# Kernel tuning notes

Measured on AMD Instinct MI355X. Metric: run time of the kernel, lower is better.

The kernel has to match this reference:

```python
import jax, jax.numpy as jnp
import numpy as np

H = 4096
DFF = 16384
EPS = 1e-5

def _layernorm(x, gamma, beta, eps):
    mu = jnp.mean(x, axis=-1, keepdims=True)
    var = jnp.var(x, axis=-1, keepdims=True)
    return (x - mu) * jax.lax.rsqrt(var + eps) * gamma + beta

def setup_inputs() -> dict:
    key = jax.random.key(0)
    ks = jax.random.split(key, 9)
    B, S = 2, 2048
    s_h = 1.0 / np.sqrt(H)
    s_f = 1.0 / np.sqrt(DFF)
    return {
        "input": jax.random.normal(ks[0], (B, S, H), jnp.float32),
        "residual": jax.random.normal(ks[1], (B, S, H), jnp.float32),
        "residual_norm": jax.random.normal(ks[2], (B, S, H), jnp.float32),
        "bias": jax.random.normal(ks[3], (H,), jnp.float32) * 0.02,
        "attn_nw": 1.0 + jax.random.normal(ks[4], (H,), jnp.float32) * 0.02,
        "attn_nb": jax.random.normal(ks[5], (H,), jnp.float32) * 0.02,
        "inter_w": jax.random.normal(ks[6], (H, DFF), jnp.float32) * s_h,
        "inter_b": jax.random.normal(ks[7], (DFF,), jnp.float32) * 0.02,
        "output_w": jax.random.normal(ks[8], (DFF, H), jnp.float32) * s_f,
        "output_b": jnp.zeros((H,), jnp.float32),
    }

def reference(input, residual, residual_norm, bias, attn_nw, attn_nb,
              inter_w, inter_b, output_w, output_b):
    # mlp_gemm (pre_layer_norm, mlp_after_attn, fp32, no quant):
    # LN(input + residual + attn_bias) -> GEMM -> GeLU -> GEMM
    ln_in = input + residual + bias                      # [B,S,H]
    ln = _layernorm(ln_in, attn_nw, attn_nb, EPS)        # [B,S,H]
    inter = jax.nn.gelu(jnp.einsum('bsh,hf->bsf', ln, inter_w) + inter_b,
                        approximate=True)                # [B,S,DFF]
    out = jnp.einsum('bsf,fh->bsh', inter, output_w)     # [B,S,H]
    # residual_add (preln, add_bias, mp_size=1):
    # residual = mlp_out + residual + attn_out + (attn_bias + mlp_bias)/mp_size
    return out + residual + input + (bias + output_b)
```

## Files before the change

kernel.cpp:

```cpp
#include <hip/hip_runtime.h>
#include <cstdint>
#include <cstddef>

#define H_DIM 4096
#define DFF_DIM 16384
#define NROWS 4096

typedef unsigned short bf16_t;
typedef __attribute__((ext_vector_type(8))) short bf16x8;
typedef __attribute__((ext_vector_type(4))) float f32x4;
typedef __attribute__((ext_vector_type(4))) unsigned short u16x4;

static __device__ __forceinline__ bf16_t f2bf(float f) {
  union { float f; unsigned int i; } v; v.f = f;
  unsigned int x = v.i;
  return (bf16_t)((x + 0x7fffu + ((x >> 16) & 1u)) >> 16);
}

#define GLDS16(gp, lp)                                                    \
  __builtin_amdgcn_global_load_lds(                                       \
      (__attribute__((address_space(1))) void*)(gp),                      \
      (__attribute__((address_space(3))) void*)(lp), 16, 0, 0)

__global__ __launch_bounds__(256) void fused_ln_kernel(
    const float* __restrict__ inp, const float* __restrict__ res,
    const float* __restrict__ bias, const float* __restrict__ gamma,
    const float* __restrict__ beta, bf16_t* __restrict__ out) {
  int row = blockIdx.x;
  int t = threadIdx.x;
  const float4* pin = (const float4*)(inp + (size_t)row * H_DIM);
  const float4* pre = (const float4*)(res + (size_t)row * H_DIM);
  const float4* pbi = (const float4*)bias;
  float4 xv[4];
  float s = 0.f, ss = 0.f;
#pragma unroll
  for (int i = 0; i < 4; ++i) {
    int idx = t + i * 256;
    float4 a = pin[idx];
    float4 b = pre[idx];
    float4 c = pbi[idx];
    float4 v;
    v.x = a.x + b.x + c.x;
    v.y = a.y + b.y + c.y;
    v.z = a.z + b.z + c.z;
    v.w = a.w + b.w + c.w;
    xv[i] = v;
    s += v.x + v.y + v.z + v.w;
    ss += v.x * v.x + v.y * v.y + v.z * v.z + v.w * v.w;
  }
#pragma unroll
  for (int off = 32; off > 0; off >>= 1) {
    s += __shfl_xor(s, off);
    ss += __shfl_xor(ss, off);
  }
  __shared__ float sred[8];
  int w = t >> 6, l = t & 63;
  if (l == 0) { sred[w] = s; sred[4 + w] = ss; }
  __syncthreads();
  s = sred[0] + sred[1] + sred[2] + sred[3];
  ss = sred[4] + sred[5] + sred[6] + sred[7];
  const float inv = 1.f / (float)H_DIM;
  float mean = s * inv;
  float var = ss * inv - mean * mean;
  float rstd = rsqrtf(var + 1e-5f);
  const float4* pg = (const float4*)gamma;
  const float4* pb = (const float4*)beta;
#pragma unroll
  for (int i = 0; i < 4; ++i) {
    int idx = t + i * 256;
    float4 g = pg[idx];
    float4 bb = pb[idx];
    float4 v = xv[i];
    u16x4 o;
    o.x = f2bf((v.x - mean) * rstd * g.x + bb.x);
    o.y = f2bf((v.y - mean) * rstd * g.y + bb.y);
    o.z = f2bf((v.z - mean) * rstd * g.z + bb.z);
    o.w = f2bf((v.w - mean) * rstd * g.w + bb.w);
    *(u16x4*)(out + (size_t)row * H_DIM + (size_t)idx * 4) = o;
  }
}

__global__ __launch_bounds__(256) void transpose_cvt_kernel(
    const float* __restrict__ W, bf16_t* __restrict__ Wt, int K, int N) {
  __shared__ float tile[64][65];
  int nb = N >> 6;
  int bk = blockIdx.x / nb;
  int bn = blockIdx.x - bk * nb;
  int t = threadIdx.x;
  int r = t >> 4;
  int c4 = (t & 15) << 2;
#pragma unroll
  for (int p = 0; p < 4; ++p) {
    int row = r + p * 16;
    float4 v = *(const float4*)(W + (size_t)(bk * 64 + row) * N + bn * 64 + c4);
    tile[row][c4 + 0] = v.x;
    tile[row][c4 + 1] = v.y;
    tile[row][c4 + 2] = v.z;
    tile[row][c4 + 3] = v.w;
  }
  __syncthreads();
#pragma unroll
  for (int p = 0; p < 4; ++p) {
    int nn = r + p * 16;
    u16x4 o;
    o.x = f2bf(tile[c4 + 0][nn]);
    o.y = f2bf(tile[c4 + 1][nn]);
    o.z = f2bf(tile[c4 + 2][nn]);
    o.w = f2bf(tile[c4 + 3][nn]);
    *(u16x4*)(Wt + (size_t)(bn * 64 + nn) * K + bk * 64 + c4) = o;
  }
}

#define QMFMA_H(AQ, BQ, MILO, NJLO, K5)                                     \
  __builtin_amdgcn_s_setprio(1);                                            \
  _Pragma("unroll") for (int i5 = 0; i5 < 4; ++i5)                          \
  _Pragma("unroll") for (int j5 = 0; j5 < 2; ++j5)                          \
    acc[MILO + i5][NJLO + j5] = __builtin_amdgcn_mfma_f32_16x16x32_bf16(    \
        AQ[i5 * 2 + K5], BQ[j5 * 2 + K5], acc[MILO + i5][NJLO + j5], 0, 0, 0); \
  __builtin_amdgcn_s_setprio(0);

#define BAR __builtin_amdgcn_s_barrier()
#define VM6 asm volatile("s_waitcnt vmcnt(6)" ::: "memory")

template <int EPI>
__global__ __launch_bounds__(512, 2) void gemm8p_kernel(
    const bf16_t* __restrict__ A, const bf16_t* __restrict__ Bt,
    int M, int N, int K,
    const float* __restrict__ eb1, const float* __restrict__ eb2,
    const float* __restrict__ add1, const float* __restrict__ add2,
    bf16_t* __restrict__ outb, float* __restrict__ outf) {
  __shared__ char lds[131072];

  const int t = threadIdx.x;
  const int l = t & 63;
  const int wid = t >> 6;
  const int wr = wid >> 2;
  const int wc = wid & 3;

  int nwg = gridDim.x;
  int bid = blockIdx.x;
  int wg = (bid & 7) * (nwg >> 3) + (bid >> 3);
  int ntm = M >> 8;
  int chunk = wg >> 5, s5 = wg & 31;
  int cmn = ntm >> 3;
  int cm = chunk % cmn, cn = chunk / cmn;
  int tm = cm * 8 + (s5 & 7);
  int tn = cn * 4 + (s5 >> 3);
  size_t m0 = (size_t)tm * 256, n0 = (size_t)tn * 256;

  f32x4 acc[8][4];
#pragma unroll
  for (int i = 0; i < 8; ++i)
#pragma unroll
    for (int j = 0; j < 4; ++j) acc[i][j] = {0.f, 0.f, 0.f, 0.f};

  const int rh = t >> 3;
  const int sl = t & 7;
  const int oc = sl ^ ((rh >> 1) & 7);
  const bf16_t* sA0 = A + (m0 + rh) * (size_t)K + oc * 8;
  const bf16_t* sA1 = A + (m0 + rh + 64) * (size_t)K + oc * 8;
  const bf16_t* sB0 = Bt + (n0 + rh) * (size_t)K + oc * 8;
  const bf16_t* sB1 = Bt + (n0 + rh + 64) * (size_t)K + oc * 8;

  auto stA = [&](int b, int h, int T) {
    GLDS16(sA0 + (size_t)h * 128 * K + (size_t)T * 64,
           lds + b * 32768 + h * 16384 + t * 16);
    GLDS16(sA1 + (size_t)h * 128 * K + (size_t)T * 64,
           lds + b * 32768 + h * 16384 + (t + 512) * 16);
  };
  auto stB = [&](int b, int h, int T) {
    GLDS16(sB0 + (size_t)h * 128 * K + (size_t)T * 64,
           lds + 65536 + b * 32768 + h * 16384 + t * 16);
    GLDS16(sB1 + (size_t)h * 128 * K + (size_t)T * 64,
           lds + 65536 + b * 32768 + h * 16384 + (t + 512) * 16);
  };

  int offA[8][2], offB[4][2];
#pragma unroll
  for (int mi = 0; mi < 8; ++mi) {
    int h = mi >> 2;
    int lr = (mi & 3) * 32 + wr * 16 + (l & 15);
#pragma unroll
    for (int ks = 0; ks < 2; ++ks) {
      int o = ks * 4 + (l >> 4);
      offA[mi][ks] = h * 16384 + lr * 128 + ((o ^ ((lr >> 1) & 7)) << 4);
    }
  }
#pragma unroll
  for (int nj = 0; nj < 4; ++nj) {
    int h = nj >> 1;
    int lc = (nj & 1) * 64 + wc * 16 + (l & 15);
#pragma unroll
    for (int ks = 0; ks < 2; ++ks) {
      int o = ks * 4 + (l >> 4);
      offB[nj][ks] = 65536 + h * 16384 + lc * 128 + ((o ^ ((lc >> 1) & 7)) << 4);
    }
  }

  auto rd8 = [&](int off) -> bf16x8 {
    return *(const bf16x8*)(const void*)(lds + off);
  };

  const int NT = K >> 6;
  const int NI = NT >> 1;

  stB(0, 0, 0); stA(0, 0, 0); stB(0, 1, 0); stA(0, 1, 0);
  stB(1, 0, 1); stA(1, 0, 1); stB(1, 1, 1);
  VM6;
  BAR;

  bf16x8 aQ[8], bQ0[4], bQ1[4];
#pragma unroll
  for (int i = 0; i < 4; ++i)
#pragma unroll
    for (int ks = 0; ks < 2; ++ks) aQ[i * 2 + ks] = rd8(offA[i][ks]);
#pragma unroll
  for (int j = 0; j < 2; ++j)
#pragma unroll
    for (int ks = 0; ks < 2; ++ks) bQ0[j * 2 + ks] = rd8(offB[j][ks]);

  for (int it = 0; it < NI; ++it) {
    const int Tb = 2 * it + 1;
    int Sa = 2 * it + 2; if (Sa >= NT) Sa = NT - 1;
    int Sb = 2 * it + 3; if (Sb >= NT) Sb = NT - 1;

    stA(1, 1, Tb);
    BAR;
    QMFMA_H(aQ, bQ0, 0, 0, 0)
    bQ1[0] = rd8(offB[2][0]); bQ1[2] = rd8(offB[3][0]);
    QMFMA_H(aQ, bQ0, 0, 0, 1)
    bQ1[1] = rd8(offB[2][1]); bQ1[3] = rd8(offB[3][1]);
    BAR;
    stB(0, 0, Sa);
    BAR;
    QMFMA_H(aQ, bQ1, 0, 2, 0)
    aQ[0] = rd8(offA[4][0]); aQ[2] = rd8(offA[5][0]);
    aQ[4] = rd8(offA[6][0]); aQ[6] = rd8(offA[7][0]);
    QMFMA_H(aQ, bQ1, 0, 2, 1)
    aQ[1] = rd8(offA[4][1]); aQ[3] = rd8(offA[5][1]);
    aQ[5] = rd8(offA[6][1]); aQ[7] = rd8(offA[7][1]);
    BAR;
    stA(0, 0, Sa);
    BAR;
    QMFMA_H(aQ, bQ1, 4, 2, 0)
    QMFMA_H(aQ, bQ1, 4, 2, 1)
    BAR;
    stB(0, 1, Sa);
    VM6;
    BAR;
    QMFMA_H(aQ, bQ0, 4, 0, 0)
    bQ0[0] = rd8(32768 + offB[0][0]); bQ0[2] = rd8(32768 + offB[1][0]);
    aQ[0] = rd8(32768 + offA[0][0]); aQ[2] = rd8(32768 + offA[1][0]);
    aQ[4] = rd8(32768 + offA[2][0]); aQ[6] = rd8(32768 + offA[3][0]);
    QMFMA_H(aQ, bQ0, 4, 0, 1)
    bQ0[1] = rd8(32768 + offB[0][1]); bQ0[3] = rd8(32768 + offB[1][1]);
    aQ[1] = rd8(32768 + offA[0][1]); aQ[3] = rd8(32768 + offA[1][1]);
    aQ[5] = rd8(32768 + offA[2][1]); aQ[7] = rd8(32768 + offA[3][1]);
    BAR;

    stA(0, 1, Sa);
    BAR;
    QMFMA_H(aQ, bQ0, 0, 0, 0)
    bQ1[0] = rd8(32768 + offB[2][0]); bQ1[2] = rd8(32768 + offB[3][0]);
    QMFMA_H(aQ, bQ0, 0, 0, 1)
    bQ1[1] = rd8(32768 + offB[2][1]); bQ1[3] = rd8(32768 + offB[3][1]);
    BAR;
    stB(1, 0, Sb);
    BAR;
    QMFMA_H(aQ, bQ1, 0, 2, 0)
    aQ[0] = rd8(32768 + offA[4][0]); aQ[2] = rd8(32768 + offA[5][0]);
    aQ[4] = rd8(32768 + offA[6][0]); aQ[6] = rd8(32768 + offA[7][0]);
    QMFMA_H(aQ, bQ1, 0, 2, 1)
    aQ[1] = rd8(32768 + offA[4][1]); aQ[3] = rd8(32768 + offA[5][1]);
    aQ[5] = rd8(32768 + offA[6][1]); aQ[7] = rd8(32768 + offA[7][1]);
    BAR;
    stA(1, 0, Sb);
    BAR;
    QMFMA_H(aQ, bQ1, 4, 2, 0)
    QMFMA_H(aQ, bQ1, 4, 2, 1)
    BAR;
    stB(1, 1, Sb);
    VM6;
    BAR;
    QMFMA_H(aQ, bQ0, 4, 0, 0)
    bQ0[0] = rd8(offB[0][0]); bQ0[2] = rd8(offB[1][0]);
    aQ[0] = rd8(offA[0][0]); aQ[2] = rd8(offA[1][0]);
    aQ[4] = rd8(offA[2][0]); aQ[6] = rd8(offA[3][0]);
    QMFMA_H(aQ, bQ0, 4, 0, 1)
    bQ0[1] = rd8(offB[0][1]); bQ0[3] = rd8(offB[1][1]);
    aQ[1] = rd8(offA[0][1]); aQ[3] = rd8(offA[1][1]);
    aQ[5] = rd8(offA[2][1]); aQ[7] = rd8(offA[3][1]);
    BAR;
  }
  asm volatile("s_waitcnt vmcnt(0)" ::: "memory");

  int lr4 = (l >> 4) * 4;
  int lc = l & 15;
#pragma unroll
  for (int mi = 0; mi < 8; ++mi) {
#pragma unroll
    for (int i2 = 0; i2 < 4; ++i2) {
      int rrow = (int)m0 + (mi * 2 + wr) * 16 + lr4 + i2;
      size_t base = (size_t)rrow * N;
#pragma unroll
      for (int nj = 0; nj < 4; ++nj) {
        int col = (int)n0 + (nj * 4 + wc) * 16 + lc;
        float v = acc[mi][nj][i2];
        if (EPI == 0) {
          float x = v + eb1[col];
          float u = 0.7978845608028654f * (x + 0.044715f * x * x * x);
          float th = 1.f - 2.f / (__expf(2.f * u) + 1.f);
          outb[base + col] = f2bf(0.5f * x * (1.f + th));
        } else {
          outf[base + col] =
              v + eb1[col] + eb2[col] + add1[base + col] + add2[base + col];
        }
      }
    }
  }
}

extern "C" void kernel_launch(void* const* d_in, const int* in_sizes, int n_in,
                              void* d_out, int out_size, void* d_ws,
                              size_t ws_size, hipStream_t stream) {
  const float* input = (const float*)d_in[0];
  const float* residual = (const float*)d_in[1];
  const float* bias = (const float*)d_in[3];
  const float* attn_nw = (const float*)d_in[4];
  const float* attn_nb = (const float*)d_in[5];
  const float* inter_w = (const float*)d_in[6];
  const float* inter_b = (const float*)d_in[7];
  const float* output_w = (const float*)d_in[8];
  const float* output_b = (const float*)d_in[9];
  float* out = (float*)d_out;

  char* ws = (char*)d_ws;
  bf16_t* lnb = (bf16_t*)ws;
  bf16_t* w1t = (bf16_t*)(ws + (size_t)NROWS * H_DIM * 2);
  bf16_t* w2t = (bf16_t*)(ws + (size_t)NROWS * H_DIM * 2 +
                          (size_t)H_DIM * DFF_DIM * 2);
  bf16_t* inter = (bf16_t*)(ws + (size_t)NROWS * H_DIM * 2 +
                            2 * (size_t)H_DIM * DFF_DIM * 2);

  fused_ln_kernel<<<NROWS, 256, 0, stream>>>(input, residual, bias, attn_nw,
                                             attn_nb, lnb);
  transpose_cvt_kernel<<<(H_DIM / 64) * (DFF_DIM / 64), 256, 0, stream>>>(
      inter_w, w1t, H_DIM, DFF_DIM);
  transpose_cvt_kernel<<<(DFF_DIM / 64) * (H_DIM / 64), 256, 0, stream>>>(
      output_w, w2t, DFF_DIM, H_DIM);
  gemm8p_kernel<0><<<(NROWS / 256) * (DFF_DIM / 256), 512, 0, stream>>>(
      lnb, w1t, NROWS, DFF_DIM, H_DIM, inter_b, nullptr, nullptr, nullptr,
      inter, nullptr);
  gemm8p_kernel<1><<<(NROWS / 256) * (H_DIM / 256), 512, 0, stream>>>(
      inter, w2t, NROWS, H_DIM, DFF_DIM, bias, output_b, residual, input,
      nullptr, out);
}
```

Measured before the change: 1.065 ms.

## Fuse output_w transpose-convert into first GEMM launch via interleaved extra blocks

The standalone transpose/bf16 conversion of output_w is folded into the first GEMM kernel. The grid is doubled, and odd blocks do the transpose work through an LDS tile while even blocks do the GEMM tiles. This removes a separate launch and lets the memory-bound transpose overlap with the compute-bound GEMM. The cost is that the transpose blocks compete for CU slots and bandwidth with the GEMM blocks, and the GEMM tile-to-block mapping and cache-friendly ordering are changed.

```diff
diff --git a/kernel.cpp b/kernel.cpp
--- a/kernel.cpp
+++ b/kernel.cpp
@@ -128,18 +128,51 @@
     int M, int N, int K,
     const float* __restrict__ eb1, const float* __restrict__ eb2,
     const float* __restrict__ add1, const float* __restrict__ add2,
-    bf16_t* __restrict__ outb, float* __restrict__ outf) {
+    bf16_t* __restrict__ outb, float* __restrict__ outf,
+    const float* __restrict__ tsrc, bf16_t* __restrict__ tdst) {
   __shared__ char lds[131072];
 
   const int t = threadIdx.x;
+  const int bid = blockIdx.x;
+
+  if (EPI == 0 && (bid & 1)) {
+    float (*tile)[65] = (float (*)[65])lds;
+    const int tb = bid >> 1;
+    const int r = t >> 3;
+    const int c0 = (t & 7) * 8;
+    for (int tau = tb; tau < (DFF_DIM / 64) * (H_DIM / 64); tau += 1024) {
+      int bk = tau >> 6;
+      int bn = tau & 63;
+      const float* src = tsrc + (size_t)(bk * 64 + r) * H_DIM + bn * 64 + c0;
+      float4 v0 = *(const float4*)src;
+      float4 v1 = *(const float4*)(src + 4);
+      tile[r][c0 + 0] = v0.x; tile[r][c0 + 1] = v0.y;
+      tile[r][c0 + 2] = v0.z; tile[r][c0 + 3] = v0.w;
+      tile[r][c0 + 4] = v1.x; tile[r][c0 + 5] = v1.y;
+      tile[r][c0 + 6] = v1.z; tile[r][c0 + 7] = v1.w;
+      __syncthreads();
+      u16x4 o0, o1;
+      o0.x = f2bf(tile[c0 + 0][r]); o0.y = f2bf(tile[c0 + 1][r]);
+      o0.z = f2bf(tile[c0 + 2][r]); o0.w = f2bf(tile[c0 + 3][r]);
+      o1.x = f2bf(tile[c0 + 4][r]); o1.y = f2bf(tile[c0 + 5][r]);
+      o1.z = f2bf(tile[c0 + 6][r]); o1.w = f2bf(tile[c0 + 7][r]);
+      bf16_t* dst = tdst + (size_t)(bn * 64 + r) * DFF_DIM + bk * 64 + c0;
+      *(u16x4*)dst = o0;
+      *(u16x4*)(dst + 4) = o1;
+      __syncthreads();
+    }
+    return;
+  }
+
   const int l = t & 63;
   const int wid = t >> 6;
   const int wr = wid >> 2;
   const int wc = wid & 3;
 
-  int nwg = gridDim.x;
-  int bid = blockIdx.x;
-  int wg = (bid & 7) * (nwg >> 3) + (bid >> 3);
+  int nT, idx;
+  if (EPI == 0) { nT = (int)gridDim.x >> 1; idx = bid >> 1; }
+  else          { nT = (int)gridDim.x;      idx = bid; }
+  int wg = (idx & 7) * (nT >> 3) + (idx >> 3);
   int ntm = M >> 8;
   int chunk = wg >> 5, s5 = wg & 31;
   int cmn = ntm >> 3;
@@ -346,12 +379,10 @@
                                              attn_nb, lnb);
   transpose_cvt_kernel<<<(H_DIM / 64) * (DFF_DIM / 64), 256, 0, stream>>>(
       inter_w, w1t, H_DIM, DFF_DIM);
-  transpose_cvt_kernel<<<(DFF_DIM / 64) * (H_DIM / 64), 256, 0, stream>>>(
-      output_w, w2t, DFF_DIM, H_DIM);
-  gemm8p_kernel<0><<<(NROWS / 256) * (DFF_DIM / 256), 512, 0, stream>>>(
+  gemm8p_kernel<0><<<2 * (NROWS / 256) * (DFF_DIM / 256), 512, 0, stream>>>(
       lnb, w1t, NROWS, DFF_DIM, H_DIM, inter_b, nullptr, nullptr, nullptr,
-      inter, nullptr);
+      inter, nullptr, output_w, w2t);
   gemm8p_kernel<1><<<(NROWS / 256) * (H_DIM / 256), 512, 0, stream>>>(
       inter, w2t, NROWS, H_DIM, DFF_DIM, bias, output_b, residual, input,
-      nullptr, out);
-}
+      nullptr, out, nullptr, nullptr);
+}
```

New measurement: 1.330 ms. +24.9%, slower.

## Fuse output-weight transpose-convert into first GEMM kernel tail

Applied to the files above, without the earlier changes.

Removes the separate transpose/bf16-convert launch for output_w and folds that work into the first GEMM kernel. Each of the 1024 GEMM workgroups prefetches its share of the fp32 weight tiles into registers before the main loop, then transposes them through LDS and writes bf16 after the epilogue. The goal is to hide the memory-bound transpose behind compute and drop a launch. In exchange it adds 64 float registers per thread in a kernel already at 2 waves/SIMD occupancy, which may cause spills or lower occupancy.

```diff
diff --git a/kernel.cpp b/kernel.cpp
--- a/kernel.cpp
+++ b/kernel.cpp
@@ -128,7 +128,8 @@
     int M, int N, int K,
     const float* __restrict__ eb1, const float* __restrict__ eb2,
     const float* __restrict__ add1, const float* __restrict__ add2,
-    bf16_t* __restrict__ outb, float* __restrict__ outf) {
+    bf16_t* __restrict__ outb, float* __restrict__ outf,
+    const float* __restrict__ tsrc, bf16_t* __restrict__ tdst) {
   __shared__ char lds[131072];
 
   const int t = threadIdx.x;
@@ -153,6 +154,20 @@
   for (int i = 0; i < 8; ++i)
 #pragma unroll
     for (int j = 0; j < 4; ++j) acc[i][j] = {0.f, 0.f, 0.f, 0.f};
+
+  const int trr = t >> 3;
+  const int trc = (t & 7) * 8;
+  float4 pv0[8], pv1[8];
+  if (EPI == 0) {
+#pragma unroll
+    for (int j = 0; j < 8; ++j) {
+      int tau = bid + j * 1024;
+      const float* src =
+          tsrc + (size_t)((tau >> 6) * 64 + trr) * H_DIM + (tau & 63) * 64 + trc;
+      pv0[j] = *(const float4*)src;
+      pv1[j] = *(const float4*)(src + 4);
+    }
+  }
 
   const int rh = t >> 3;
   const int sl = t & 7;
@@ -318,6 +333,39 @@
       }
     }
   }
+
+  if (EPI == 0) {
+    __syncthreads();
+    float (*tl0)[65] = (float (*)[65])(void*)lds;
+    float (*tl1)[65] = (float (*)[65])(void*)(lds + 16640);
+#pragma unroll
+    for (int j = 0; j < 16; ++j) {
+      float (*cur)[65] = (j & 1) ? tl1 : tl0;
+      float4 q0 = pv0[j & 7], q1 = pv1[j & 7];
+      cur[trr][trc + 0] = q0.x; cur[trr][trc + 1] = q0.y;
+      cur[trr][trc + 2] = q0.z; cur[trr][trc + 3] = q0.w;
+      cur[trr][trc + 4] = q1.x; cur[trr][trc + 5] = q1.y;
+      cur[trr][trc + 6] = q1.z; cur[trr][trc + 7] = q1.w;
+      if (j < 8) {
+        int tau2 = bid + (j + 8) * 1024;
+        const float* s2 = tsrc + (size_t)((tau2 >> 6) * 64 + trr) * H_DIM +
+                          (tau2 & 63) * 64 + trc;
+        pv0[j] = *(const float4*)s2;
+        pv1[j] = *(const float4*)(s2 + 4);
+      }
+      __syncthreads();
+      int tau = bid + j * 1024;
+      int bk = tau >> 6, bn = tau & 63;
+      u16x4 o0, o1;
+      o0.x = f2bf(cur[trc + 0][trr]); o0.y = f2bf(cur[trc + 1][trr]);
+      o0.z = f2bf(cur[trc + 2][trr]); o0.w = f2bf(cur[trc + 3][trr]);
+      o1.x = f2bf(cur[trc + 4][trr]); o1.y = f2bf(cur[trc + 5][trr]);
+      o1.z = f2bf(cur[trc + 6][trr]); o1.w = f2bf(cur[trc + 7][trr]);
+      bf16_t* dst = tdst + (size_t)(bn * 64 + trr) * DFF_DIM + bk * 64 + trc;
+      *(u16x4*)dst = o0;
+      *(u16x4*)(dst + 4) = o1;
+    }
+  }
 }
 
 extern "C" void kernel_launch(void* const* d_in, const int* in_sizes, int n_in,
@@ -346,12 +394,10 @@
                                              attn_nb, lnb);
   transpose_cvt_kernel<<<(H_DIM / 64) * (DFF_DIM / 64), 256, 0, stream>>>(
       inter_w, w1t, H_DIM, DFF_DIM);
-  transpose_cvt_kernel<<<(DFF_DIM / 64) * (H_DIM / 64), 256, 0, stream>>>(
-      output_w, w2t, DFF_DIM, H_DIM);
   gemm8p_kernel<0><<<(NROWS / 256) * (DFF_DIM / 256), 512, 0, stream>>>(
       lnb, w1t, NROWS, DFF_DIM, H_DIM, inter_b, nullptr, nullptr, nullptr,
-      inter, nullptr);
+      inter, nullptr, output_w, w2t);
   gemm8p_kernel<1><<<(NROWS / 256) * (H_DIM / 256), 512, 0, stream>>>(
       inter, w2t, NROWS, H_DIM, DFF_DIM, bias, output_b, residual, input,
-      nullptr, out);
+      nullptr, out, nullptr, nullptr);
 }
```

New measurement: 1.083 ms (median of 3 runs). Within noise of the previous version (+1.7%).
